# Performance work log

Measured on AMD Instinct MI355X. Metric: run time of the kernel, lower is better.

The kernel has to match this reference:

```python
import jax, jax.numpy as jnp
import numpy as np


def setup_inputs() -> dict:
    key = jax.random.key(0)
    k1, k2 = jax.random.split(key)
    x = jax.random.normal(k1, (4096, 1024), dtype=jnp.float32)  # [B, D] queries
    y = jax.random.normal(k2, (8192, 1024), dtype=jnp.float32)  # [N, D] database
    return {"x": x, "y": y}


def reference(x, y):
    # -sum((x[:, None, :] - y[None, :, :])**2, -1)  computed via the
    x_sq = jnp.sum(x * x, axis=-1)              # [B]
    y_sq = jnp.sum(y * y, axis=-1)              # [N]
    xy = jnp.einsum('bd,nd->bn', x, y)          # [B, N]
    return -(x_sq[:, None] - 2.0 * xy + y_sq[None, :])  # [B, N]
```

## Files before the change

### kernel.cpp

```cpp
#include <hip/hip_runtime.h>
#include <hip/hip_bf16.h>


typedef __attribute__((ext_vector_type(4))) int i32x4;

#define BM 256
#define BN 256
#define KD 1024
#define NT 8

__device__ __forceinline__ void gld16(const void* g, void* l) {
    __builtin_amdgcn_global_load_lds(
        (const __attribute__((address_space(1))) unsigned int*)g,
        (__attribute__((address_space(3))) unsigned int*)l,
        16, 0, 0);
}

__global__ __launch_bounds__(256) void prep_q(
    const float* __restrict__ x, const float* __restrict__ y,
    signed char* __restrict__ xq, signed char* __restrict__ yq,
    float* __restrict__ sx, float* __restrict__ sy,
    float* __restrict__ xsq, float* __restrict__ ysq, int M, int N)
{
    int row = blockIdx.x;
    const float* src;
    signed char* dst;
    float* nrm;
    float* scl;
    float sfac;
    if (row < M) {
        src = x + (size_t)row * KD; dst = xq + (size_t)row * KD;
        nrm = xsq + row; scl = sx + row; sfac = 2.0f;
    } else {
        int r = row - M;
        src = y + (size_t)r * KD; dst = yq + (size_t)r * KD;
        nrm = ysq + r; scl = sy + r; sfac = 1.0f;
    }
    int t = threadIdx.x;
    float4 v = ((const float4*)src)[t];
    float ss = v.x * v.x + v.y * v.y + v.z * v.z + v.w * v.w;
    float am = fmaxf(fmaxf(fabsf(v.x), fabsf(v.y)),
                     fmaxf(fabsf(v.z), fabsf(v.w)));
    #pragma unroll
    for (int off = 32; off > 0; off >>= 1) {
        ss += __shfl_down(ss, off, 64);
        am = fmaxf(am, __shfl_down(am, off, 64));
    }
    __shared__ float rs[4], rm[4];
    if ((t & 63) == 0) { rs[t >> 6] = ss; rm[t >> 6] = am; }
    __syncthreads();
    float tots = rs[0] + rs[1] + rs[2] + rs[3];
    float totm = fmaxf(fmaxf(rm[0], rm[1]), fmaxf(rm[2], rm[3]));
    float inv = totm > 0.0f ? 127.0f / totm : 0.0f;

    int q0 = (int)rintf(v.x * inv), q1 = (int)rintf(v.y * inv);
    int q2 = (int)rintf(v.z * inv), q3 = (int)rintf(v.w * inv);
    q0 = max(-127, min(127, q0)); q1 = max(-127, min(127, q1));
    q2 = max(-127, min(127, q2)); q3 = max(-127, min(127, q3));
    int packed = (q0 & 255) | ((q1 & 255) << 8) |
                 ((q2 & 255) << 16) | ((q3 & 255) << 24);
    ((int*)dst)[t] = packed;
    if (t == 0) { *nrm = tots; *scl = sfac * totm / 127.0f; }
}

__global__ __launch_bounds__(1024, 4) void gemm_i8(
    const signed char* __restrict__ xq, const signed char* __restrict__ yq,
    const float* __restrict__ sx, const float* __restrict__ sy,
    const float* __restrict__ xsq, const float* __restrict__ ysq,
    float* __restrict__ out, int M, int N)
{
    __shared__ __align__(16) char lds[131072];

    const int ntm = M / BM;
    const int ntn = N / BN;
    const int bid = blockIdx.x;
    int tm, tn;
    if (ntm == 16 && ntn == 32) {
        int xcd = bid & 7, k = bid >> 3;
        tm = (xcd >> 2) * 8 + (k >> 3);
        tn = (xcd & 3) * 8 + (k & 7);
    } else {
        tm = bid / ntn;
        tn = bid % ntn;
    }

    const int tid  = threadIdx.x;
    const int wid  = tid >> 6;
    const int lane = tid & 63;
    const int wr   = wid >> 2;
    const int wc   = wid & 3;
    const int l15  = lane & 15;
    const int hi   = lane >> 4;

    const int r128 = tid >> 3;
    const int cbs  = (tid & 7) ^ (r128 & 7);
    const signed char* aBase = xq + (size_t)(tm * BM + r128) * KD + cbs * 16;
    const signed char* bBase = yq + (size_t)(tn * BN + r128) * KD + cbs * 16;
    const int dstB = tid * 16;

    #define STAGE(kt, buf) do {                                               \
        const signed char* ga_ = aBase + (size_t)(kt) * 128;                  \
        const signed char* gb_ = bBase + (size_t)(kt) * 128;                  \
        char* da_ = &lds[(buf) * 32768 + dstB];                               \
        char* db_ = &lds[65536 + (buf) * 32768 + dstB];                       \
        gld16(ga_, da_); gld16(ga_ + 128 * KD, da_ + 16384);                  \
        gld16(gb_, db_); gld16(gb_ + 128 * KD, db_ + 16384);                  \
    } while (0)

    int aro[4], bro[4], xk[2];
    #pragma unroll
    for (int mi = 0; mi < 4; ++mi) aro[mi] = (wr * 64 + mi * 16 + l15) * 128;
    #pragma unroll
    for (int nj = 0; nj < 4; ++nj) bro[nj] = (wc * 64 + nj * 16 + l15) * 128;
    xk[0] = ((0 + hi) ^ (l15 & 7)) * 16;
    xk[1] = ((4 + hi) ^ (l15 & 7)) * 16;

    i32x4 acc[4][4] = {};

    STAGE(0, 0);
    __syncthreads();

    int buf = 0;
    for (int t = 0; t < NT; ++t) {
        if (t + 1 < NT) STAGE(t + 1, buf ^ 1);
        const int ab = buf * 32768;

        #pragma unroll
        for (int ks = 0; ks < 2; ++ks) {
            i32x4 aF[4], bF[4];
            #pragma unroll
            for (int mi = 0; mi < 4; ++mi)
                aF[mi] = *(const i32x4*)&lds[ab + aro[mi] + xk[ks]];
            #pragma unroll
            for (int nj = 0; nj < 4; ++nj)
                bF[nj] = *(const i32x4*)&lds[65536 + ab + bro[nj] + xk[ks]];
            __builtin_amdgcn_s_setprio(1);
            #pragma unroll
            for (int mi = 0; mi < 4; ++mi)
                #pragma unroll
                for (int nj = 0; nj < 4; ++nj)
                    acc[mi][nj] = __builtin_amdgcn_mfma_i32_16x16x64_i8(
                        aF[mi], bF[nj], acc[mi][nj], 0, 0, 0);
            __builtin_amdgcn_s_setprio(0);
        }
        __syncthreads();
        buf ^= 1;
    }

    #pragma unroll
    for (int mi = 0; mi < 4; ++mi) {
        int r0 = tm * BM + wr * 64 + mi * 16 + hi * 4;
        #pragma unroll
        for (int nj = 0; nj < 4; ++nj) {
            int c = tn * BN + wc * 64 + nj * 16 + l15;
            float syv = sy[c];
            float ysv = ysq[c];
            #pragma unroll
            for (int r = 0; r < 4; ++r) {
                int row = r0 + r;
                out[(size_t)row * N + c] =
                    sx[row] * syv * (float)acc[mi][nj][r] - xsq[row] - ysv;
            }
        }
    }
}

__global__ __launch_bounds__(256) void fallback_l2(
    const float* __restrict__ x, const float* __restrict__ y,
    float* __restrict__ out, int M, int N, int K)
{
    int tx = threadIdx.x & 15, ty = threadIdx.x >> 4;
    int row = blockIdx.y * 16 + ty;
    int col = blockIdx.x * 16 + tx;
    __shared__ float xs[16][17], ys[16][17];
    float s = 0.f;
    for (int k0 = 0; k0 < K; k0 += 16) {
        xs[ty][tx] = x[(size_t)row * K + k0 + tx];
        ys[ty][tx] = y[(size_t)(blockIdx.x * 16 + ty) * K + k0 + tx];
        __syncthreads();
        #pragma unroll
        for (int kk = 0; kk < 16; ++kk) {
            float d = xs[ty][kk] - ys[tx][kk];
            s += d * d;
        }
        __syncthreads();
    }
    out[(size_t)row * N + col] = -s;
}

extern "C" void kernel_launch(void* const* d_in, const int* in_sizes, int n_in,
                              void* d_out, int out_size, void* d_ws, size_t ws_size,
                              hipStream_t stream) {
    const float* x = (const float*)d_in[0];
    const float* y = (const float*)d_in[1];
    float* out = (float*)d_out;
    const int M = in_sizes[0] / KD;
    const int N = in_sizes[1] / KD;

    size_t need = (size_t)(M + N) * KD
                + (size_t)(M + N) * 2 * sizeof(float) + 256;
    if (ws_size >= need && M == 4096 && N == 8192) {
        char* w = (char*)d_ws;
        signed char* xq = (signed char*)w;
        signed char* yq = xq + (size_t)M * KD;
        float* sx  = (float*)(yq + (size_t)N * KD);
        float* sy  = sx + M;
        float* xsq = sy + N;
        float* ysq = xsq + M;

        prep_q<<<M + N, 256, 0, stream>>>(x, y, xq, yq, sx, sy, xsq, ysq, M, N);
        int grid = (M / BM) * (N / BN);
        gemm_i8<<<grid, 1024, 0, stream>>>(xq, yq, sx, sy, xsq, ysq, out, M, N);
    } else {
        dim3 g(N / 16, M / 16);
        fallback_l2<<<g, 256, 0, stream>>>(x, y, out, M, N, KD);
    }
}
```

Before: 67.25 us.

## Shrink int8 GEMM tiles to 128x128 with 256-thread blocks and K-step 64

Moves the int8 MFMA GEMM from 256x256 output tiles with 16 waves and 128-byte K slices to 128x128 tiles with 4 waves and 64-byte K slices. LDS use drops from 128KB to 32KB per block, so several blocks can share a CU, and the grid grows from 512 to 2048 blocks. The XCD-aware tile mapping and LDS swizzle are adjusted to match. In exchange, each block reuses less data, so global and L2 traffic for the quantized inputs roughly doubles, and there are twice as many K iterations, each with its own barrier.

```diff
diff --git a/kernel.cpp b/kernel.cpp
--- a/kernel.cpp
+++ b/kernel.cpp
@@ -4,10 +4,8 @@
 
 typedef __attribute__((ext_vector_type(4))) int i32x4;
 
-#define BM 256
-#define BN 256
 #define KD 1024
-#define NT 8
+#define NT 16
 
 __device__ __forceinline__ void gld16(const void* g, void* l) {
     __builtin_amdgcn_global_load_lds(
@@ -63,22 +61,22 @@
     if (t == 0) { *nrm = tots; *scl = sfac * totm / 127.0f; }
 }
 
-__global__ __launch_bounds__(1024, 4) void gemm_i8(
+__global__ __launch_bounds__(256, 4) void gemm_i8(
     const signed char* __restrict__ xq, const signed char* __restrict__ yq,
     const float* __restrict__ sx, const float* __restrict__ sy,
     const float* __restrict__ xsq, const float* __restrict__ ysq,
     float* __restrict__ out, int M, int N)
 {
-    __shared__ __align__(16) char lds[131072];
-
-    const int ntm = M / BM;
-    const int ntn = N / BN;
+    __shared__ __align__(16) char lds[32768];
+
+    const int ntm = M / 128;
+    const int ntn = N / 128;
     const int bid = blockIdx.x;
     int tm, tn;
-    if (ntm == 16 && ntn == 32) {
+    if (ntm == 32 && ntn == 64) {
         int xcd = bid & 7, k = bid >> 3;
-        tm = (xcd >> 2) * 8 + (k >> 3);
-        tn = (xcd & 3) * 8 + (k & 7);
+        tm = (xcd >> 1) * 8 + (k >> 5);
+        tn = (xcd & 1) * 32 + (k & 31);
     } else {
         tm = bid / ntn;
         tn = bid % ntn;
@@ -87,33 +85,32 @@
     const int tid  = threadIdx.x;
     const int wid  = tid >> 6;
     const int lane = tid & 63;
-    const int wr   = wid >> 2;
-    const int wc   = wid & 3;
+    const int wr   = wid >> 1;
+    const int wc   = wid & 1;
     const int l15  = lane & 15;
     const int hi   = lane >> 4;
 
-    const int r128 = tid >> 3;
-    const int cbs  = (tid & 7) ^ (r128 & 7);
-    const signed char* aBase = xq + (size_t)(tm * BM + r128) * KD + cbs * 16;
-    const signed char* bBase = yq + (size_t)(tn * BN + r128) * KD + cbs * 16;
+    const int srow = tid >> 2;
+    const int cbs  = (tid & 3) ^ (srow & 3);
+    const signed char* aBase = xq + (size_t)(tm * 128 + srow) * KD + cbs * 16;
+    const signed char* bBase = yq + (size_t)(tn * 128 + srow) * KD + cbs * 16;
     const int dstB = tid * 16;
 
     #define STAGE(kt, buf) do {                                               \
-        const signed char* ga_ = aBase + (size_t)(kt) * 128;                  \
-        const signed char* gb_ = bBase + (size_t)(kt) * 128;                  \
-        char* da_ = &lds[(buf) * 32768 + dstB];                               \
-        char* db_ = &lds[65536 + (buf) * 32768 + dstB];                       \
-        gld16(ga_, da_); gld16(ga_ + 128 * KD, da_ + 16384);                  \
-        gld16(gb_, db_); gld16(gb_ + 128 * KD, db_ + 16384);                  \
+        const signed char* ga_ = aBase + (size_t)(kt) * 64;                   \
+        const signed char* gb_ = bBase + (size_t)(kt) * 64;                   \
+        char* da_ = &lds[(buf) * 8192 + dstB];                                \
+        char* db_ = &lds[16384 + (buf) * 8192 + dstB];                        \
+        gld16(ga_, da_); gld16(ga_ + 64 * KD, da_ + 4096);                    \
+        gld16(gb_, db_); gld16(gb_ + 64 * KD, db_ + 4096);                    \
     } while (0)
 
-    int aro[4], bro[4], xk[2];
-    #pragma unroll
-    for (int mi = 0; mi < 4; ++mi) aro[mi] = (wr * 64 + mi * 16 + l15) * 128;
-    #pragma unroll
-    for (int nj = 0; nj < 4; ++nj) bro[nj] = (wc * 64 + nj * 16 + l15) * 128;
-    xk[0] = ((0 + hi) ^ (l15 & 7)) * 16;
-    xk[1] = ((4 + hi) ^ (l15 & 7)) * 16;
+    int aro[4], bro[4];
+    #pragma unroll
+    for (int mi = 0; mi < 4; ++mi) aro[mi] = (wr * 64 + mi * 16 + l15) * 64;
+    #pragma unroll
+    for (int nj = 0; nj < 4; ++nj) bro[nj] = (wc * 64 + nj * 16 + l15) * 64;
+    const int xk = (hi ^ (l15 & 3)) * 16;
 
     i32x4 acc[4][4] = {};
 
@@ -123,36 +120,33 @@
     int buf = 0;
     for (int t = 0; t < NT; ++t) {
         if (t + 1 < NT) STAGE(t + 1, buf ^ 1);
-        const int ab = buf * 32768;
-
-        #pragma unroll
-        for (int ks = 0; ks < 2; ++ks) {
-            i32x4 aF[4], bF[4];
-            #pragma unroll
-            for (int mi = 0; mi < 4; ++mi)
-                aF[mi] = *(const i32x4*)&lds[ab + aro[mi] + xk[ks]];
+        const int ab = buf * 8192;
+
+        i32x4 aF[4], bF[4];
+        #pragma unroll
+        for (int mi = 0; mi < 4; ++mi)
+            aF[mi] = *(const i32x4*)&lds[ab + aro[mi] + xk];
+        #pragma unroll
+        for (int nj = 0; nj < 4; ++nj)
+            bF[nj] = *(const i32x4*)&lds[16384 + ab + bro[nj] + xk];
+        __builtin_amdgcn_s_setprio(1);
+        #pragma unroll
+        for (int mi = 0; mi < 4; ++mi)
             #pragma unroll
             for (int nj = 0; nj < 4; ++nj)
-                bF[nj] = *(const i32x4*)&lds[65536 + ab + bro[nj] + xk[ks]];
-            __builtin_amdgcn_s_setprio(1);
-            #pragma unroll
-            for (int mi = 0; mi < 4; ++mi)
-                #pragma unroll
-                for (int nj = 0; nj < 4; ++nj)
-                    acc[mi][nj] = __builtin_amdgcn_mfma_i32_16x16x64_i8(
-                        aF[mi], bF[nj], acc[mi][nj], 0, 0, 0);
-            __builtin_amdgcn_s_setprio(0);
-        }
+                acc[mi][nj] = __builtin_amdgcn_mfma_i32_16x16x64_i8(
+                    aF[mi], bF[nj], acc[mi][nj], 0, 0, 0);
+        __builtin_amdgcn_s_setprio(0);
         __syncthreads();
         buf ^= 1;
     }
 
     #pragma unroll
     for (int mi = 0; mi < 4; ++mi) {
-        int r0 = tm * BM + wr * 64 + mi * 16 + hi * 4;
+        int r0 = tm * 128 + wr * 64 + mi * 16 + hi * 4;
         #pragma unroll
         for (int nj = 0; nj < 4; ++nj) {
-            int c = tn * BN + wc * 64 + nj * 16 + l15;
+            int c = tn * 128 + wc * 64 + nj * 16 + l15;
             float syv = sy[c];
             float ysv = ysq[c];
             #pragma unroll
@@ -209,8 +203,8 @@
         float* ysq = xsq + M;
 
         prep_q<<<M + N, 256, 0, stream>>>(x, y, xq, yq, sx, sy, xsq, ysq, M, N);
-        int grid = (M / BM) * (N / BN);
-        gemm_i8<<<grid, 1024, 0, stream>>>(xq, yq, sx, sy, xsq, ysq, out, M, N);
+        int grid = (M / 128) * (N / 128);
+        gemm_i8<<<grid, 256, 0, stream>>>(xq, yq, sx, sy, xsq, ysq, out, M, N);
     } else {
         dim3 g(N / 16, M / 16);
         fallback_l2<<<g, 256, 0, stream>>>(x, y, out, M, N, KD);
```

Result: slower. 76.51 us (+13.8%).
